# Kernel optimization log

Hardware: AMD Instinct MI355X
Metric: run time of the kernel (lower is better)

Reference implementation:

```python
import jax, jax.numpy as jnp
import numpy as np

N = 200000    # nodes
DMAX = 32     # max in-degree (padded)
F = 128       # in_feats
H = 128       # lstm hidden == in_feats (use_pp=False)
OUT = 128     # out_feats


def setup_inputs() -> dict:
    key = jax.random.key(0)
    ks = jax.random.split(key, 11)
    u = lambda k, shape, s: jax.random.uniform(k, shape, jnp.float32, -s, s)
    feat = jax.random.normal(ks[0], (N, F), jnp.float32)
    # norms come from sqrt(degree) in the original; keep them positive, O(1)
    in_norm = jax.random.uniform(ks[1], (N,), jnp.float32) + 1.0
    out_norm = jax.random.uniform(ks[2], (N,), jnp.float32) + 1.0
    neighbors = jax.random.randint(ks[3], (N, DMAX), 0, N, jnp.int32)
    degrees = jax.random.randint(ks[4], (N,), 1, DMAX + 1, jnp.int32)
    s_lstm = 1.0 / np.sqrt(H)   # torch LSTM default init scale
    s_lin = 1.0 / np.sqrt(F)    # module's reset_parameters scale
    W_ih = u(ks[5], (4 * H, F), s_lstm)
    W_hh = u(ks[6], (4 * H, H), s_lstm)
    b_ih = u(ks[7], (4 * H,), s_lstm)
    b_hh = u(ks[8], (4 * H,), s_lstm)
    W_lin = u(ks[9], (OUT, F), s_lin)
    b_lin = u(ks[10], (OUT,), s_lin)
    return dict(feat=feat, in_norm=in_norm, out_norm=out_norm,
                W_ih=W_ih, W_hh=W_hh, b_ih=b_ih, b_hh=b_hh,
                W_lin=W_lin, b_lin=b_lin,
                neighbors=neighbors, degrees=degrees)


def reference(feat, in_norm, out_norm, W_ih, W_hh, b_ih, b_hh, W_lin, b_lin,
              neighbors, degrees):
    # graph.nodes['_U'].data['h'] = feat / out_norm
    msg_src = feat / out_norm[:, None]                      # [N, F]
    n, dmax = neighbors.shape
    h_dim = W_hh.shape[1]
    step_mask = jnp.arange(dmax)[None, :] < degrees[:, None]  # [N, DMAX]

    def step(carry, xs):
        h, c = carry
        idx_t, m_t = xs                                      # [N], [N]
        x = msg_src[idx_t]                                   # gather messages [N, F]
        gates = x @ W_ih.T + b_ih + h @ W_hh.T + b_hh        # [N, 4H]
        i, f, g, o = jnp.split(gates, 4, axis=-1)
        i = jax.nn.sigmoid(i)
        f = jax.nn.sigmoid(f)
        o = jax.nn.sigmoid(o)
        g = jnp.tanh(g)
        c_new = f * c + i * g
        h_new = o * jnp.tanh(c_new)
        m = m_t[:, None]
        return (jnp.where(m, h_new, h), jnp.where(m, c_new, c)), None

    init = (jnp.zeros((n, h_dim), feat.dtype), jnp.zeros((n, h_dim), feat.dtype))
    (h_final, _), _ = jax.lax.scan(step, init, (neighbors.T, step_mask.T))
    # feat = linear(h / in_norm)
    return (h_final / in_norm[:, None]) @ W_lin.T + b_lin
```

## Files before the change

### kernel.cpp

```cpp
#include <hip/hip_runtime.h>

#define NN 200000
#define NB 64
#define NWG (NN / NB)

typedef unsigned short u16;
typedef unsigned int u32;
typedef __attribute__((ext_vector_type(8))) short short8;
typedef __attribute__((ext_vector_type(4))) float f32x4;

#define LOG2E 1.4426950408889634f
#define TWOLOG2E 2.8853900817779268f

__device__ __forceinline__ u16 f2bf(float x) {
  u32 u = __float_as_uint(x);
  u += 0x7FFFu + ((u >> 16) & 1u);
  return (u16)(u >> 16);
}

typedef __attribute__((address_space(3))) unsigned int lds_u32_t;
typedef const __attribute__((address_space(1))) unsigned int glb_u32_t;
__device__ __forceinline__ void gload16(const void* g, void* l) {
  __builtin_amdgcn_global_load_lds((glb_u32_t*)g, (lds_u32_t*)l, 16, 0, 0);
}

__global__ void k_prep_msg(const float* __restrict__ feat, const float* __restrict__ onorm,
                           u16* __restrict__ msg) {
  int i = blockIdx.x * 256 + threadIdx.x;
  int row = i >> 4, c8 = (i & 15) * 8;
  const float4 a = *(const float4*)(feat + (size_t)row * 128 + c8);
  const float4 b = *(const float4*)(feat + (size_t)row * 128 + c8 + 4);
  float s = 1.0f / onorm[row];
  short8 v = { (short)f2bf(a.x * s), (short)f2bf(a.y * s), (short)f2bf(a.z * s), (short)f2bf(a.w * s),
               (short)f2bf(b.x * s), (short)f2bf(b.y * s), (short)f2bf(b.z * s), (short)f2bf(b.w * s) };
  *(short8*)(msg + (size_t)row * 128 + c8) = v;
}

__global__ void k_prep_w(const float* __restrict__ Wih, const float* __restrict__ Whh,
                         const float* __restrict__ Wlin, const float* __restrict__ bih,
                         const float* __restrict__ bhh, u16* __restrict__ wihb,
                         u16* __restrict__ whhb, u16* __restrict__ wlinb,
                         float* __restrict__ bsum) {
  int i = blockIdx.x * 256 + threadIdx.x;
  if (i < 65536) {
    int gate = i >> 14;
    float s = (gate == 2) ? TWOLOG2E : -LOG2E;
    wihb[i] = f2bf(Wih[i] * s);
  } else if (i < 131072) {
    int j = i - 65536;
    int gate = j >> 14;
    float s = (gate == 2) ? TWOLOG2E : -LOG2E;
    whhb[j] = f2bf(Whh[j] * s);
  } else if (i < 147456) {
    wlinb[i - 131072] = f2bf(Wlin[i - 131072]);
  } else {
    int j = i - 147456;
    float s = ((j >> 7) == 2) ? TWOLOG2E : -LOG2E;
    bsum[j] = (bih[j] + bhh[j]) * s;
  }
}

__global__ void k_hist(const int* __restrict__ degs, int* __restrict__ hist, int n) {
  __shared__ int lh[33];
  if (threadIdx.x < 33) lh[threadIdx.x] = 0;
  __syncthreads();
  int i = blockIdx.x * 256 + threadIdx.x;
  if (i < n) atomicAdd(&lh[degs[i]], 1);
  __syncthreads();
  if (threadIdx.x < 33 && lh[threadIdx.x]) atomicAdd(&hist[threadIdx.x], lh[threadIdx.x]);
}

__global__ void k_scan(const int* __restrict__ hist, int* __restrict__ basep) {
  if (threadIdx.x == 0 && blockIdx.x == 0) {
    int a = 0;
    for (int d = 32; d >= 1; --d) { basep[d] = a; a += hist[d]; }
    basep[0] = a;
  }
}

__global__ void k_scatter(const int* __restrict__ degs, int* __restrict__ basep,
                          int* __restrict__ perm, int n) {
  __shared__ int lh[33], lbase[33], lc[33];
  int t = threadIdx.x;
  if (t < 33) { lh[t] = 0; lc[t] = 0; }
  __syncthreads();
  int i = blockIdx.x * 256 + t;
  int d = (i < n) ? degs[i] : 0;
  if (i < n) atomicAdd(&lh[d], 1);
  __syncthreads();
  if (t < 33 && lh[t]) lbase[t] = atomicAdd(&basep[t], lh[t]);
  __syncthreads();
  if (i < n) { int r = atomicAdd(&lc[d], 1); perm[lbase[d] + r] = i; }
}

__global__ __launch_bounds__(512, 2) void k_main(
    const u16* __restrict__ msg, const u16* __restrict__ wihb,
    const u16* __restrict__ whhb, const u16* __restrict__ wlinb,
    const float* __restrict__ bsum, const float* __restrict__ blin,
    const float* __restrict__ inorm, const int* __restrict__ nbrs,
    const int* __restrict__ degs, const int* __restrict__ perm,
    float* __restrict__ out) {
  __shared__ alignas(16) u16 Xl[2][64 * 128];
  __shared__ alignas(16) u16 Hl[2][64 * 136];
  __shared__ int gidl[64];

  const int tid = threadIdx.x;
  const int w = tid >> 6;
  const int lane = tid & 63;
  const int l15 = lane & 15;
  const int g4 = lane >> 4;
  const int w16 = w * 16;
  const int gr = tid >> 4;
  const int xc8 = (((tid & 15) ^ (gr & 15)) * 8);
  const int wbase = w * 512;
  const int base = blockIdx.x * NB;

  if (tid < NB) gidl[tid] = perm[base + tid];
  {
    u32* hz = (u32*)Hl[0];
#pragma unroll
    for (int s = 0; s < 8; ++s) hz[tid + s * 512] = 0;
    if (tid < 256) hz[tid + 4096] = 0;
  }
  __syncthreads();

  const int gid0 = gidl[gr], gid1 = gidl[gr + 32];
  const int* nb0 = nbrs + (size_t)gid0 * 32;
  const int* nb1 = nbrs + (size_t)gid1 * 32;

  {
    int i0 = nb0[0], i1 = nb1[0];
    gload16(msg + (size_t)i0 * 128 + xc8, &Xl[0][wbase]);
    gload16(msg + (size_t)i1 * 128 + xc8, &Xl[0][4096 + wbase]);
  }
  int ni0 = 0, ni1 = 0;
  if (degs[gidl[0]] > 1) { ni0 = nb0[1]; ni1 = nb1[1]; }

  short8 fih[4][4], fhh[4][4];
#pragma unroll
  for (int g = 0; g < 4; ++g)
#pragma unroll
    for (int kk = 0; kk < 4; ++kk) {
      size_t o = (size_t)(g * 128 + w16 + l15) * 128 + kk * 32 + g4 * 8;
      fih[g][kk] = *(const short8*)(wihb + o);
      fhh[g][kk] = *(const short8*)(whhb + o);
    }
  float bias[4];
#pragma unroll
  for (int g = 0; g < 4; ++g) bias[g] = bsum[g * 128 + w16 + l15];

  u32 dgp[4];
#pragma unroll
  for (int r = 0; r < 4; ++r) {
    u32 p = 0;
#pragma unroll
    for (int q = 0; q < 4; ++q) p |= ((u32)degs[gidl[r * 16 + g4 * 4 + q]]) << (8 * q);
    dgp[r] = p;
  }
  const int maxdeg = degs[gidl[0]];

  int xsw[4];
#pragma unroll
  for (int kk = 0; kk < 4; ++kk) xsw[kk] = ((kk * 4 + g4) ^ l15) * 8;

  float c[4][4] = {};
  u32 hpk[4][2] = {};
  __syncthreads();

  int cur = 0;
  for (int t = 0; t < maxdeg; ++t) {
    const int nxt = cur ^ 1;
    if (t + 1 < maxdeg) {
      gload16(msg + (size_t)ni0 * 128 + xc8, &Xl[nxt][wbase]);
      gload16(msg + (size_t)ni1 * 128 + xc8, &Xl[nxt][4096 + wbase]);
    }
    if (t + 2 < maxdeg) { ni0 = nb0[t + 2]; ni1 = nb1[t + 2]; }

    const u16* Xc = &Xl[cur][0];
    const u16* Hc = &Hl[cur][0];
    u16* Hn = &Hl[nxt][0];

#pragma unroll
    for (int rp = 0; rp < 2; ++rp) {
      f32x4 acc[2][4];
#pragma unroll
      for (int r = 0; r < 2; ++r)
#pragma unroll
        for (int g = 0; g < 4; ++g) acc[r][g] = (f32x4){bias[g], bias[g], bias[g], bias[g]};

#pragma unroll
      for (int rf = 0; rf < 2; ++rf) {
        short8 ax[4];
#pragma unroll
        for (int kk = 0; kk < 4; ++kk)
          ax[kk] = *(const short8*)(&Xc[(rp * 32 + rf * 16 + l15) * 128 + xsw[kk]]);
#pragma unroll
        for (int kk = 0; kk < 4; ++kk)
#pragma unroll
          for (int g = 0; g < 4; ++g)
            acc[rf][g] = __builtin_amdgcn_mfma_f32_16x16x32_bf16(ax[kk], fih[g][kk], acc[rf][g], 0, 0, 0);
      }
#pragma unroll
      for (int rf = 0; rf < 2; ++rf) {
        short8 ah[4];
#pragma unroll
        for (int kk = 0; kk < 4; ++kk)
          ah[kk] = *(const short8*)(&Hc[(rp * 32 + rf * 16 + l15) * 136 + kk * 32 + g4 * 8]);
#pragma unroll
        for (int kk = 0; kk < 4; ++kk)
#pragma unroll
          for (int g = 0; g < 4; ++g)
            acc[rf][g] = __builtin_amdgcn_mfma_f32_16x16x32_bf16(ah[kk], fhh[g][kk], acc[rf][g], 0, 0, 0);
      }

#pragma unroll
      for (int r = 0; r < 2; ++r) {
        const int rr = rp * 2 + r;
#pragma unroll
        for (int q = 0; q < 4; ++q) {
          float ei = __builtin_amdgcn_exp2f(acc[r][0][q]);
          float ef = __builtin_amdgcn_exp2f(acc[r][1][q]);
          float eg = __builtin_amdgcn_exp2f(acc[r][2][q]);
          float eo = __builtin_amdgcn_exp2f(acc[r][3][q]);
          float fv  = __builtin_amdgcn_rcpf(1.0f + ef);
          float rig = __builtin_amdgcn_rcpf((1.0f + ei) * (1.0f + eg));
          float ig  = (eg - 1.0f) * rig;
          float cn  = fv * c[rr][q] + ig;
          float ec  = __builtin_amdgcn_exp2f(cn * TWOLOG2E);
          float rho = __builtin_amdgcn_rcpf((1.0f + eo) * (1.0f + ec));
          float hn  = (ec - 1.0f) * rho;
          bool act = (int)((dgp[rr] >> (8 * q)) & 255u) > t;
          c[rr][q] = act ? cn : c[rr][q];
          u32 word = hpk[rr][q >> 1];
          u16 oldv = (u16)(word >> ((q & 1) * 16));
          u16 nh = act ? f2bf(hn) : oldv;
          hpk[rr][q >> 1] = (q & 1) ? ((word & 0x0000FFFFu) | ((u32)nh << 16))
                                    : ((word & 0xFFFF0000u) | (u32)nh);
          Hn[(rr * 16 + g4 * 4 + q) * 136 + w16 + l15] = nh;
        }
      }
    }
    __syncthreads();
    cur = nxt;
  }

  const u16* Hf = &Hl[cur][0];

  short8 wl[4];
#pragma unroll
  for (int kk = 0; kk < 4; ++kk)
    wl[kk] = *(const short8*)(wlinb + (size_t)(w16 + l15) * 128 + kk * 32 + g4 * 8);
  f32x4 a2[4] = {};
#pragma unroll
  for (int kk = 0; kk < 4; ++kk)
#pragma unroll
    for (int r = 0; r < 4; ++r) {
      short8 ah = *(const short8*)(&Hf[(r * 16 + l15) * 136 + kk * 32 + g4 * 8]);
      a2[r] = __builtin_amdgcn_mfma_f32_16x16x32_bf16(ah, wl[kk], a2[r], 0, 0, 0);
    }
  float blv = blin[w16 + l15];
#pragma unroll
  for (int r = 0; r < 4; ++r)
#pragma unroll
    for (int q = 0; q < 4; ++q) {
      int nl = r * 16 + g4 * 4 + q;
      int g = gidl[nl];
      out[(size_t)g * 128 + w16 + l15] = a2[r][q] / inorm[g] + blv;
    }
}

extern "C" void kernel_launch(void* const* d_in, const int* in_sizes, int n_in,
                              void* d_out, int out_size, void* d_ws, size_t ws_size,
                              hipStream_t stream) {
  const float* feat    = (const float*)d_in[0];
  const float* in_norm = (const float*)d_in[1];
  const float* out_nrm = (const float*)d_in[2];
  const float* W_ih    = (const float*)d_in[3];
  const float* W_hh    = (const float*)d_in[4];
  const float* b_ih    = (const float*)d_in[5];
  const float* b_hh    = (const float*)d_in[6];
  const float* W_lin   = (const float*)d_in[7];
  const float* b_lin   = (const float*)d_in[8];
  const int* neighbors = (const int*)d_in[9];
  const int* degrees   = (const int*)d_in[10];
  float* out = (float*)d_out;

  char* ws = (char*)d_ws;
  u16* msg    = (u16*)(ws);
  u16* wihb   = (u16*)(ws + 51200000);
  u16* whhb   = (u16*)(ws + 51331072);
  u16* wlinb  = (u16*)(ws + 51462144);
  float* bsum = (float*)(ws + 51494912);
  int* perm   = (int*)(ws + 51496960);
  int* hist   = (int*)(ws + 52296960);
  int* basep  = hist + 64;
  if (ws_size < 52297600) return;

  hipMemsetAsync(hist, 0, 64 * 4, stream);
  k_prep_msg<<<12500, 256, 0, stream>>>(feat, out_nrm, msg);
  k_prep_w<<<578, 256, 0, stream>>>(W_ih, W_hh, W_lin, b_ih, b_hh, wihb, whhb, wlinb, bsum);
  k_hist<<<782, 256, 0, stream>>>(degrees, hist, NN);
  k_scan<<<1, 1, 0, stream>>>(hist, basep);
  k_scatter<<<782, 256, 0, stream>>>(degrees, basep, perm, NN);
  k_main<<<NWG, 512, 0, stream>>>(msg, wihb, whhb, wlinb, bsum, b_lin, in_norm,
                                  neighbors, degrees, perm, out);
}
```

Measured before the change: 1.059 ms.

## Split node tile into two half-tiles with independent buffers and per-half max degree

Each 64-node workgroup now runs as two 32-row halves with separate X/H double buffers and separate step counts. The second half stops once its own maximum degree is reached instead of running to the tile-wide maximum. Each half's MFMA block is wrapped in s_setprio raises so waves prioritize matrix work. The cost is an extra barrier per timestep and duplicated code, which raises register and instruction pressure.

```diff
diff --git a/kernel.cpp b/kernel.cpp
--- a/kernel.cpp
+++ b/kernel.cpp
@@ -100,8 +100,10 @@
     const float* __restrict__ inorm, const int* __restrict__ nbrs,
     const int* __restrict__ degs, const int* __restrict__ perm,
     float* __restrict__ out) {
-  __shared__ alignas(16) u16 Xl[2][64 * 128];
-  __shared__ alignas(16) u16 Hl[2][64 * 136];
+  __shared__ alignas(16) u16 XA[2][32 * 128];
+  __shared__ alignas(16) u16 XB[2][32 * 128];
+  __shared__ alignas(16) u16 HA[2][32 * 136];
+  __shared__ alignas(16) u16 HB[2][32 * 136];
   __shared__ int gidl[64];
 
   const int tid = threadIdx.x;
@@ -117,24 +119,22 @@
 
   if (tid < NB) gidl[tid] = perm[base + tid];
   {
-    u32* hz = (u32*)Hl[0];
-#pragma unroll
-    for (int s = 0; s < 8; ++s) hz[tid + s * 512] = 0;
-    if (tid < 256) hz[tid + 4096] = 0;
-  }
-  __syncthreads();
-
-  const int gid0 = gidl[gr], gid1 = gidl[gr + 32];
-  const int* nb0 = nbrs + (size_t)gid0 * 32;
-  const int* nb1 = nbrs + (size_t)gid1 * 32;
-
-  {
-    int i0 = nb0[0], i1 = nb1[0];
-    gload16(msg + (size_t)i0 * 128 + xc8, &Xl[0][wbase]);
-    gload16(msg + (size_t)i1 * 128 + xc8, &Xl[0][4096 + wbase]);
-  }
-  int ni0 = 0, ni1 = 0;
-  if (degs[gidl[0]] > 1) { ni0 = nb0[1]; ni1 = nb1[1]; }
+    u32* a = (u32*)HA[0];
+    u32* b = (u32*)HB[0];
+#pragma unroll
+    for (int s = 0; s < 4; ++s) { a[tid + s * 512] = 0; b[tid + s * 512] = 0; }
+    if (tid < 128) { a[tid + 2048] = 0; b[tid + 2048] = 0; }
+  }
+  __syncthreads();
+
+  const int gidA = gidl[gr], gidB = gidl[32 + gr];
+  const int* nbA = nbrs + (size_t)gidA * 32;
+  const int* nbB = nbrs + (size_t)gidB * 32;
+
+  gload16(msg + (size_t)nbA[0] * 128 + xc8, &XA[0][wbase]);
+  gload16(msg + (size_t)nbB[0] * 128 + xc8, &XB[0][wbase]);
+  int niA = nbA[1];
+  int niB = nbB[1];
 
   short8 fih[4][4], fhh[4][4];
 #pragma unroll
@@ -149,51 +149,53 @@
 #pragma unroll
   for (int g = 0; g < 4; ++g) bias[g] = bsum[g * 128 + w16 + l15];
 
-  u32 dgp[4];
-#pragma unroll
-  for (int r = 0; r < 4; ++r) {
-    u32 p = 0;
-#pragma unroll
-    for (int q = 0; q < 4; ++q) p |= ((u32)degs[gidl[r * 16 + g4 * 4 + q]]) << (8 * q);
-    dgp[r] = p;
-  }
-  const int maxdeg = degs[gidl[0]];
+  u32 dgpA[2], dgpB[2];
+#pragma unroll
+  for (int r = 0; r < 2; ++r) {
+    u32 pa = 0, pb = 0;
+#pragma unroll
+    for (int q = 0; q < 4; ++q) {
+      pa |= ((u32)degs[gidl[r * 16 + g4 * 4 + q]]) << (8 * q);
+      pb |= ((u32)degs[gidl[32 + r * 16 + g4 * 4 + q]]) << (8 * q);
+    }
+    dgpA[r] = pa; dgpB[r] = pb;
+  }
+  const int maxdegA = degs[gidl[0]];
+  const int maxdegB = degs[gidl[32]];
 
   int xsw[4];
 #pragma unroll
   for (int kk = 0; kk < 4; ++kk) xsw[kk] = ((kk * 4 + g4) ^ l15) * 8;
 
-  float c[4][4] = {};
-  u32 hpk[4][2] = {};
-  __syncthreads();
-
-  int cur = 0;
-  for (int t = 0; t < maxdeg; ++t) {
-    const int nxt = cur ^ 1;
-    if (t + 1 < maxdeg) {
-      gload16(msg + (size_t)ni0 * 128 + xc8, &Xl[nxt][wbase]);
-      gload16(msg + (size_t)ni1 * 128 + xc8, &Xl[nxt][4096 + wbase]);
-    }
-    if (t + 2 < maxdeg) { ni0 = nb0[t + 2]; ni1 = nb1[t + 2]; }
-
-    const u16* Xc = &Xl[cur][0];
-    const u16* Hc = &Hl[cur][0];
-    u16* Hn = &Hl[nxt][0];
-
-#pragma unroll
-    for (int rp = 0; rp < 2; ++rp) {
+  float cA[2][4] = {}, cB[2][4] = {};
+  u32 hpkA[2][2] = {}, hpkB[2][2] = {};
+  __syncthreads();
+
+  for (int t = 0; t < maxdegA; ++t) {
+    const int curb = t & 1, nxtb = curb ^ 1;
+
+    {
+      if (t + 1 < maxdegA)
+        gload16(msg + (size_t)niA * 128 + xc8, &XA[nxtb][wbase]);
+      niA = nbA[(t + 2) <= 31 ? (t + 2) : 31];
+
+      const u16* Xc = &XA[curb][0];
+      const u16* Hc = &HA[curb][0];
+      u16* Hn = &HA[nxtb][0];
+
       f32x4 acc[2][4];
 #pragma unroll
       for (int r = 0; r < 2; ++r)
 #pragma unroll
         for (int g = 0; g < 4; ++g) acc[r][g] = (f32x4){bias[g], bias[g], bias[g], bias[g]};
 
+      __builtin_amdgcn_s_setprio(1);
 #pragma unroll
       for (int rf = 0; rf < 2; ++rf) {
         short8 ax[4];
 #pragma unroll
         for (int kk = 0; kk < 4; ++kk)
-          ax[kk] = *(const short8*)(&Xc[(rp * 32 + rf * 16 + l15) * 128 + xsw[kk]]);
+          ax[kk] = *(const short8*)(&Xc[(rf * 16 + l15) * 128 + xsw[kk]]);
 #pragma unroll
         for (int kk = 0; kk < 4; ++kk)
 #pragma unroll
@@ -205,67 +207,139 @@
         short8 ah[4];
 #pragma unroll
         for (int kk = 0; kk < 4; ++kk)
-          ah[kk] = *(const short8*)(&Hc[(rp * 32 + rf * 16 + l15) * 136 + kk * 32 + g4 * 8]);
+          ah[kk] = *(const short8*)(&Hc[(rf * 16 + l15) * 136 + kk * 32 + g4 * 8]);
 #pragma unroll
         for (int kk = 0; kk < 4; ++kk)
 #pragma unroll
           for (int g = 0; g < 4; ++g)
             acc[rf][g] = __builtin_amdgcn_mfma_f32_16x16x32_bf16(ah[kk], fhh[g][kk], acc[rf][g], 0, 0, 0);
       }
-
-#pragma unroll
-      for (int r = 0; r < 2; ++r) {
-        const int rr = rp * 2 + r;
+      __builtin_amdgcn_s_setprio(0);
+
+#pragma unroll
+      for (int rr = 0; rr < 2; ++rr)
 #pragma unroll
         for (int q = 0; q < 4; ++q) {
-          float ei = __builtin_amdgcn_exp2f(acc[r][0][q]);
-          float ef = __builtin_amdgcn_exp2f(acc[r][1][q]);
-          float eg = __builtin_amdgcn_exp2f(acc[r][2][q]);
-          float eo = __builtin_amdgcn_exp2f(acc[r][3][q]);
+          float ei = __builtin_amdgcn_exp2f(acc[rr][0][q]);
+          float ef = __builtin_amdgcn_exp2f(acc[rr][1][q]);
+          float eg = __builtin_amdgcn_exp2f(acc[rr][2][q]);
+          float eo = __builtin_amdgcn_exp2f(acc[rr][3][q]);
           float fv  = __builtin_amdgcn_rcpf(1.0f + ef);
           float rig = __builtin_amdgcn_rcpf((1.0f + ei) * (1.0f + eg));
           float ig  = (eg - 1.0f) * rig;
-          float cn  = fv * c[rr][q] + ig;
+          float cn  = fv * cA[rr][q] + ig;
           float ec  = __builtin_amdgcn_exp2f(cn * TWOLOG2E);
           float rho = __builtin_amdgcn_rcpf((1.0f + eo) * (1.0f + ec));
           float hn  = (ec - 1.0f) * rho;
-          bool act = (int)((dgp[rr] >> (8 * q)) & 255u) > t;
-          c[rr][q] = act ? cn : c[rr][q];
-          u32 word = hpk[rr][q >> 1];
+          bool act = (int)((dgpA[rr] >> (8 * q)) & 255u) > t;
+          cA[rr][q] = act ? cn : cA[rr][q];
+          u32 word = hpkA[rr][q >> 1];
           u16 oldv = (u16)(word >> ((q & 1) * 16));
           u16 nh = act ? f2bf(hn) : oldv;
-          hpk[rr][q >> 1] = (q & 1) ? ((word & 0x0000FFFFu) | ((u32)nh << 16))
-                                    : ((word & 0xFFFF0000u) | (u32)nh);
+          hpkA[rr][q >> 1] = (q & 1) ? ((word & 0x0000FFFFu) | ((u32)nh << 16))
+                                     : ((word & 0xFFFF0000u) | (u32)nh);
           Hn[(rr * 16 + g4 * 4 + q) * 136 + w16 + l15] = nh;
         }
+    }
+    __syncthreads();
+
+    if (t < maxdegB) {
+      if (t + 1 < maxdegB)
+        gload16(msg + (size_t)niB * 128 + xc8, &XB[nxtb][wbase]);
+      niB = nbB[(t + 2) <= 31 ? (t + 2) : 31];
+
+      const u16* Xc = &XB[curb][0];
+      const u16* Hc = &HB[curb][0];
+      u16* Hn = &HB[nxtb][0];
+
+      f32x4 acc[2][4];
+#pragma unroll
+      for (int r = 0; r < 2; ++r)
+#pragma unroll
+        for (int g = 0; g < 4; ++g) acc[r][g] = (f32x4){bias[g], bias[g], bias[g], bias[g]};
+
+      __builtin_amdgcn_s_setprio(1);
+#pragma unroll
+      for (int rf = 0; rf < 2; ++rf) {
+        short8 ax[4];
+#pragma unroll
+        for (int kk = 0; kk < 4; ++kk)
+          ax[kk] = *(const short8*)(&Xc[(rf * 16 + l15) * 128 + xsw[kk]]);
+#pragma unroll
+        for (int kk = 0; kk < 4; ++kk)
+#pragma unroll
+          for (int g = 0; g < 4; ++g)
+            acc[rf][g] = __builtin_amdgcn_mfma_f32_16x16x32_bf16(ax[kk], fih[g][kk], acc[rf][g], 0, 0, 0);
       }
+#pragma unroll
+      for (int rf = 0; rf < 2; ++rf) {
+        short8 ah[4];
+#pragma unroll
+        for (int kk = 0; kk < 4; ++kk)
+          ah[kk] = *(const short8*)(&Hc[(rf * 16 + l15) * 136 + kk * 32 + g4 * 8]);
+#pragma unroll
+        for (int kk = 0; kk < 4; ++kk)
+#pragma unroll
+          for (int g = 0; g < 4; ++g)
+            acc[rf][g] = __builtin_amdgcn_mfma_f32_16x16x32_bf16(ah[kk], fhh[g][kk], acc[rf][g], 0, 0, 0);
+      }
+      __builtin_amdgcn_s_setprio(0);
+
+#pragma unroll
+      for (int rr = 0; rr < 2; ++rr)
+#pragma unroll
+        for (int q = 0; q < 4; ++q) {
+          float ei = __builtin_amdgcn_exp2f(acc[rr][0][q]);
+          float ef = __builtin_amdgcn_exp2f(acc[rr][1][q]);
+          float eg = __builtin_amdgcn_exp2f(acc[rr][2][q]);
+          float eo = __builtin_amdgcn_exp2f(acc[rr][3][q]);
+          float fv  = __builtin_amdgcn_rcpf(1.0f + ef);
+          float rig = __builtin_amdgcn_rcpf((1.0f + ei) * (1.0f + eg));
+          float ig  = (eg - 1.0f) * rig;
+          float cn  = fv * cB[rr][q] + ig;
+          float ec  = __builtin_amdgcn_exp2f(cn * TWOLOG2E);
+          float rho = __builtin_amdgcn_rcpf((1.0f + eo) * (1.0f + ec));
+          float hn  = (ec - 1.0f) * rho;
+          bool act = (int)((dgpB[rr] >> (8 * q)) & 255u) > t;
+          cB[rr][q] = act ? cn : cB[rr][q];
+          u32 word = hpkB[rr][q >> 1];
+          u16 oldv = (u16)(word >> ((q & 1) * 16));
+          u16 nh = act ? f2bf(hn) : oldv;
+          hpkB[rr][q >> 1] = (q & 1) ? ((word & 0x0000FFFFu) | ((u32)nh << 16))
+                                     : ((word & 0xFFFF0000u) | (u32)nh);
+          Hn[(rr * 16 + g4 * 4 + q) * 136 + w16 + l15] = nh;
+        }
     }
     __syncthreads();
-    cur = nxt;
-  }
-
-  const u16* Hf = &Hl[cur][0];
+  }
+
+  const u16* HfA = &HA[maxdegA & 1][0];
+  const u16* HfB = &HB[maxdegB & 1][0];
 
   short8 wl[4];
 #pragma unroll
   for (int kk = 0; kk < 4; ++kk)
     wl[kk] = *(const short8*)(wlinb + (size_t)(w16 + l15) * 128 + kk * 32 + g4 * 8);
-  f32x4 a2[4] = {};
+  f32x4 aA[2] = {}, aB[2] = {};
 #pragma unroll
   for (int kk = 0; kk < 4; ++kk)
 #pragma unroll
-    for (int r = 0; r < 4; ++r) {
-      short8 ah = *(const short8*)(&Hf[(r * 16 + l15) * 136 + kk * 32 + g4 * 8]);
-      a2[r] = __builtin_amdgcn_mfma_f32_16x16x32_bf16(ah, wl[kk], a2[r], 0, 0, 0);
+    for (int r = 0; r < 2; ++r) {
+      short8 hA = *(const short8*)(&HfA[(r * 16 + l15) * 136 + kk * 32 + g4 * 8]);
+      short8 hB = *(const short8*)(&HfB[(r * 16 + l15) * 136 + kk * 32 + g4 * 8]);
+      aA[r] = __builtin_amdgcn_mfma_f32_16x16x32_bf16(hA, wl[kk], aA[r], 0, 0, 0);
+      aB[r] = __builtin_amdgcn_mfma_f32_16x16x32_bf16(hB, wl[kk], aB[r], 0, 0, 0);
     }
   float blv = blin[w16 + l15];
 #pragma unroll
-  for (int r = 0; r < 4; ++r)
+  for (int r = 0; r < 2; ++r)
 #pragma unroll
     for (int q = 0; q < 4; ++q) {
       int nl = r * 16 + g4 * 4 + q;
-      int g = gidl[nl];
-      out[(size_t)g * 128 + w16 + l15] = a2[r][q] / inorm[g] + blv;
+      int gA = gidl[nl];
+      int gB = gidl[32 + nl];
+      out[(size_t)gA * 128 + w16 + l15] = aA[r][q] / inorm[gA] + blv;
+      out[(size_t)gB * 128 + w16 + l15] = aB[r][q] / inorm[gB] + blv;
     }
 }
 
```

Measured after the change: 1.183 ms. +11.7%, slower.

## Replace per-step block barriers with LDS flag counters and triple-buffered gathers

Applied to the files above, without the earlier changes.

Each timestep's __syncthreads is replaced by per-step LDS counters that each of the 8 waves increments after finishing its writes. Waves spin on a flag only when they need the gathered X tile or the previous H tile. The X buffer becomes triple-buffered, with gathers issued two steps ahead, so the input projection for the first half of the rows can start before the previous step's H is complete. MFMA sections are bracketed with s_setprio. This aims to cut barrier stalls and hide gather latency, at the cost of busy-wait spinning and fragile memory-ordering assumptions.

```diff
diff --git a/kernel.cpp b/kernel.cpp
--- a/kernel.cpp
+++ b/kernel.cpp
@@ -22,6 +22,11 @@
 typedef const __attribute__((address_space(1))) unsigned int glb_u32_t;
 __device__ __forceinline__ void gload16(const void* g, void* l) {
   __builtin_amdgcn_global_load_lds((glb_u32_t*)g, (lds_u32_t*)l, 16, 0, 0);
+}
+
+__device__ __forceinline__ void spin8(const volatile int* p) {
+  while (*p < 8) { }
+  asm volatile("" ::: "memory");
 }
 
 __global__ void k_prep_msg(const float* __restrict__ feat, const float* __restrict__ onorm,
@@ -100,9 +105,10 @@
     const float* __restrict__ inorm, const int* __restrict__ nbrs,
     const int* __restrict__ degs, const int* __restrict__ perm,
     float* __restrict__ out) {
-  __shared__ alignas(16) u16 Xl[2][64 * 128];
-  __shared__ alignas(16) u16 Hl[2][64 * 136];
+  __shared__ alignas(16) u16 Xb[3][64 * 128];
+  __shared__ alignas(16) u16 Hb[2][64 * 136];
   __shared__ int gidl[64];
+  __shared__ int fl[72];
 
   const int tid = threadIdx.x;
   const int w = tid >> 6;
@@ -114,10 +120,13 @@
   const int xc8 = (((tid & 15) ^ (gr & 15)) * 8);
   const int wbase = w * 512;
   const int base = blockIdx.x * NB;
+  volatile int* hr = fl;
+  volatile int* xr = fl + 36;
 
   if (tid < NB) gidl[tid] = perm[base + tid];
+  if (tid < 72) fl[tid] = (tid == 0) ? 8 : 0;
   {
-    u32* hz = (u32*)Hl[0];
+    u32* hz = (u32*)Hb[1];
 #pragma unroll
     for (int s = 0; s < 8; ++s) hz[tid + s * 512] = 0;
     if (tid < 256) hz[tid + 4096] = 0;
@@ -128,13 +137,11 @@
   const int* nb0 = nbrs + (size_t)gid0 * 32;
   const int* nb1 = nbrs + (size_t)gid1 * 32;
 
-  {
-    int i0 = nb0[0], i1 = nb1[0];
-    gload16(msg + (size_t)i0 * 128 + xc8, &Xl[0][wbase]);
-    gload16(msg + (size_t)i1 * 128 + xc8, &Xl[0][4096 + wbase]);
-  }
-  int ni0 = 0, ni1 = 0;
-  if (degs[gidl[0]] > 1) { ni0 = nb0[1]; ni1 = nb1[1]; }
+  gload16(msg + (size_t)nb0[0] * 128 + xc8, &Xb[0][wbase]);
+  gload16(msg + (size_t)nb1[0] * 128 + xc8, &Xb[0][4096 + wbase]);
+  gload16(msg + (size_t)nb0[1] * 128 + xc8, &Xb[1][wbase]);
+  gload16(msg + (size_t)nb1[1] * 128 + xc8, &Xb[1][4096 + wbase]);
+  int ni0 = nb0[2], ni1 = nb1[2];
 
   short8 fih[4][4], fhh[4][4];
 #pragma unroll
@@ -165,86 +172,149 @@
 
   float c[4][4] = {};
   u32 hpk[4][2] = {};
-  __syncthreads();
-
-  int cur = 0;
+
+  asm volatile("s_waitcnt vmcnt(0)" ::: "memory");
+  if (lane == 0) { atomicAdd((int*)&xr[0], 1); atomicAdd((int*)&xr[1], 1); }
+
   for (int t = 0; t < maxdeg; ++t) {
-    const int nxt = cur ^ 1;
-    if (t + 1 < maxdeg) {
-      gload16(msg + (size_t)ni0 * 128 + xc8, &Xl[nxt][wbase]);
-      gload16(msg + (size_t)ni1 * 128 + xc8, &Xl[nxt][4096 + wbase]);
-    }
-    if (t + 2 < maxdeg) { ni0 = nb0[t + 2]; ni1 = nb1[t + 2]; }
-
-    const u16* Xc = &Xl[cur][0];
-    const u16* Hc = &Hl[cur][0];
-    u16* Hn = &Hl[nxt][0];
-
-#pragma unroll
-    for (int rp = 0; rp < 2; ++rp) {
-      f32x4 acc[2][4];
-#pragma unroll
-      for (int r = 0; r < 2; ++r)
-#pragma unroll
-        for (int g = 0; g < 4; ++g) acc[r][g] = (f32x4){bias[g], bias[g], bias[g], bias[g]};
-
-#pragma unroll
-      for (int rf = 0; rf < 2; ++rf) {
-        short8 ax[4];
-#pragma unroll
-        for (int kk = 0; kk < 4; ++kk)
-          ax[kk] = *(const short8*)(&Xc[(rp * 32 + rf * 16 + l15) * 128 + xsw[kk]]);
-#pragma unroll
-        for (int kk = 0; kk < 4; ++kk)
-#pragma unroll
-          for (int g = 0; g < 4; ++g)
-            acc[rf][g] = __builtin_amdgcn_mfma_f32_16x16x32_bf16(ax[kk], fih[g][kk], acc[rf][g], 0, 0, 0);
+    const u16* Xc = &Xb[t % 3][0];
+    const u16* Hc = &Hb[(t + 1) & 1][0];
+    u16* Hn = &Hb[t & 1][0];
+
+    spin8(&xr[t]);
+    f32x4 acc[2][4];
+#pragma unroll
+    for (int r = 0; r < 2; ++r)
+#pragma unroll
+      for (int g = 0; g < 4; ++g) acc[r][g] = (f32x4){bias[g], bias[g], bias[g], bias[g]};
+    __builtin_amdgcn_s_setprio(1);
+#pragma unroll
+    for (int rf = 0; rf < 2; ++rf) {
+      short8 ax[4];
+#pragma unroll
+      for (int kk = 0; kk < 4; ++kk)
+        ax[kk] = *(const short8*)(&Xc[(rf * 16 + l15) * 128 + xsw[kk]]);
+#pragma unroll
+      for (int kk = 0; kk < 4; ++kk)
+#pragma unroll
+        for (int g = 0; g < 4; ++g)
+          acc[rf][g] = __builtin_amdgcn_mfma_f32_16x16x32_bf16(ax[kk], fih[g][kk], acc[rf][g], 0, 0, 0);
+    }
+    __builtin_amdgcn_s_setprio(0);
+
+    spin8(&hr[t]);
+
+    if (t + 2 < maxdeg) {
+      gload16(msg + (size_t)ni0 * 128 + xc8, &Xb[(t + 2) % 3][wbase]);
+      gload16(msg + (size_t)ni1 * 128 + xc8, &Xb[(t + 2) % 3][4096 + wbase]);
+    }
+    { int nt = (t + 3) <= 31 ? (t + 3) : 31; ni0 = nb0[nt]; ni1 = nb1[nt]; }
+
+    __builtin_amdgcn_s_setprio(1);
+#pragma unroll
+    for (int rf = 0; rf < 2; ++rf) {
+      short8 ah[4];
+#pragma unroll
+      for (int kk = 0; kk < 4; ++kk)
+        ah[kk] = *(const short8*)(&Hc[(rf * 16 + l15) * 136 + kk * 32 + g4 * 8]);
+#pragma unroll
+      for (int kk = 0; kk < 4; ++kk)
+#pragma unroll
+        for (int g = 0; g < 4; ++g)
+          acc[rf][g] = __builtin_amdgcn_mfma_f32_16x16x32_bf16(ah[kk], fhh[g][kk], acc[rf][g], 0, 0, 0);
+    }
+    __builtin_amdgcn_s_setprio(0);
+#pragma unroll
+    for (int r = 0; r < 2; ++r)
+#pragma unroll
+      for (int q = 0; q < 4; ++q) {
+        float ei = __builtin_amdgcn_exp2f(acc[r][0][q]);
+        float ef = __builtin_amdgcn_exp2f(acc[r][1][q]);
+        float eg = __builtin_amdgcn_exp2f(acc[r][2][q]);
+        float eo = __builtin_amdgcn_exp2f(acc[r][3][q]);
+        float fv  = __builtin_amdgcn_rcpf(1.0f + ef);
+        float rig = __builtin_amdgcn_rcpf((1.0f + ei) * (1.0f + eg));
+        float ig  = (eg - 1.0f) * rig;
+        float cn  = fv * c[r][q] + ig;
+        float ec  = __builtin_amdgcn_exp2f(cn * TWOLOG2E);
+        float rho = __builtin_amdgcn_rcpf((1.0f + eo) * (1.0f + ec));
+        float hn  = (ec - 1.0f) * rho;
+        bool act = (int)((dgp[r] >> (8 * q)) & 255u) > t;
+        c[r][q] = act ? cn : c[r][q];
+        u32 word = hpk[r][q >> 1];
+        u16 oldv = (u16)(word >> ((q & 1) * 16));
+        u16 nh = act ? f2bf(hn) : oldv;
+        hpk[r][q >> 1] = (q & 1) ? ((word & 0x0000FFFFu) | ((u32)nh << 16))
+                                 : ((word & 0xFFFF0000u) | (u32)nh);
+        Hn[(r * 16 + g4 * 4 + q) * 136 + w16 + l15] = nh;
       }
-#pragma unroll
-      for (int rf = 0; rf < 2; ++rf) {
-        short8 ah[4];
-#pragma unroll
-        for (int kk = 0; kk < 4; ++kk)
-          ah[kk] = *(const short8*)(&Hc[(rp * 32 + rf * 16 + l15) * 136 + kk * 32 + g4 * 8]);
-#pragma unroll
-        for (int kk = 0; kk < 4; ++kk)
-#pragma unroll
-          for (int g = 0; g < 4; ++g)
-            acc[rf][g] = __builtin_amdgcn_mfma_f32_16x16x32_bf16(ah[kk], fhh[g][kk], acc[rf][g], 0, 0, 0);
+
+#pragma unroll
+    for (int r = 0; r < 2; ++r)
+#pragma unroll
+      for (int g = 0; g < 4; ++g) acc[r][g] = (f32x4){bias[g], bias[g], bias[g], bias[g]};
+    __builtin_amdgcn_s_setprio(1);
+#pragma unroll
+    for (int rf = 0; rf < 2; ++rf) {
+      short8 ax[4];
+#pragma unroll
+      for (int kk = 0; kk < 4; ++kk)
+        ax[kk] = *(const short8*)(&Xc[(32 + rf * 16 + l15) * 128 + xsw[kk]]);
+#pragma unroll
+      for (int kk = 0; kk < 4; ++kk)
+#pragma unroll
+        for (int g = 0; g < 4; ++g)
+          acc[rf][g] = __builtin_amdgcn_mfma_f32_16x16x32_bf16(ax[kk], fih[g][kk], acc[rf][g], 0, 0, 0);
+    }
+#pragma unroll
+    for (int rf = 0; rf < 2; ++rf) {
+      short8 ah[4];
+#pragma unroll
+      for (int kk = 0; kk < 4; ++kk)
+        ah[kk] = *(const short8*)(&Hc[(32 + rf * 16 + l15) * 136 + kk * 32 + g4 * 8]);
+#pragma unroll
+      for (int kk = 0; kk < 4; ++kk)
+#pragma unroll
+        for (int g = 0; g < 4; ++g)
+          acc[rf][g] = __builtin_amdgcn_mfma_f32_16x16x32_bf16(ah[kk], fhh[g][kk], acc[rf][g], 0, 0, 0);
+    }
+    __builtin_amdgcn_s_setprio(0);
+#pragma unroll
+    for (int r = 0; r < 2; ++r) {
+      const int rr = 2 + r;
+#pragma unroll
+      for (int q = 0; q < 4; ++q) {
+        float ei = __builtin_amdgcn_exp2f(acc[r][0][q]);
+        float ef = __builtin_amdgcn_exp2f(acc[r][1][q]);
+        float eg = __builtin_amdgcn_exp2f(acc[r][2][q]);
+        float eo = __builtin_amdgcn_exp2f(acc[r][3][q]);
+        float fv  = __builtin_amdgcn_rcpf(1.0f + ef);
+        float rig = __builtin_amdgcn_rcpf((1.0f + ei) * (1.0f + eg));
+        float ig  = (eg - 1.0f) * rig;
+        float cn  = fv * c[rr][q] + ig;
+        float ec  = __builtin_amdgcn_exp2f(cn * TWOLOG2E);
+        float rho = __builtin_amdgcn_rcpf((1.0f + eo) * (1.0f + ec));
+        float hn  = (ec - 1.0f) * rho;
+        bool act = (int)((dgp[rr] >> (8 * q)) & 255u) > t;
+        c[rr][q] = act ? cn : c[rr][q];
+        u32 word = hpk[rr][q >> 1];
+        u16 oldv = (u16)(word >> ((q & 1) * 16));
+        u16 nh = act ? f2bf(hn) : oldv;
+        hpk[rr][q >> 1] = (q & 1) ? ((word & 0x0000FFFFu) | ((u32)nh << 16))
+                                  : ((word & 0xFFFF0000u) | (u32)nh);
+        Hn[((rr) * 16 + g4 * 4 + q) * 136 + w16 + l15] = nh;
       }
-
-#pragma unroll
-      for (int r = 0; r < 2; ++r) {
-        const int rr = rp * 2 + r;
-#pragma unroll
-        for (int q = 0; q < 4; ++q) {
-          float ei = __builtin_amdgcn_exp2f(acc[r][0][q]);
-          float ef = __builtin_amdgcn_exp2f(acc[r][1][q]);
-          float eg = __builtin_amdgcn_exp2f(acc[r][2][q]);
-          float eo = __builtin_amdgcn_exp2f(acc[r][3][q]);
-          float fv  = __builtin_amdgcn_rcpf(1.0f + ef);
-          float rig = __builtin_amdgcn_rcpf((1.0f + ei) * (1.0f + eg));
-          float ig  = (eg - 1.0f) * rig;
-          float cn  = fv * c[rr][q] + ig;
-          float ec  = __builtin_amdgcn_exp2f(cn * TWOLOG2E);
-          float rho = __builtin_amdgcn_rcpf((1.0f + eo) * (1.0f + ec));
-          float hn  = (ec - 1.0f) * rho;
-          bool act = (int)((dgp[rr] >> (8 * q)) & 255u) > t;
-          c[rr][q] = act ? cn : c[rr][q];
-          u32 word = hpk[rr][q >> 1];
-          u16 oldv = (u16)(word >> ((q & 1) * 16));
-          u16 nh = act ? f2bf(hn) : oldv;
-          hpk[rr][q >> 1] = (q & 1) ? ((word & 0x0000FFFFu) | ((u32)nh << 16))
-                                    : ((word & 0xFFFF0000u) | (u32)nh);
-          Hn[(rr * 16 + g4 * 4 + q) * 136 + w16 + l15] = nh;
-        }
-      }
-    }
-    __syncthreads();
-    cur = nxt;
-  }
-
-  const u16* Hf = &Hl[cur][0];
+    }
+
+    asm volatile("s_waitcnt vmcnt(0) lgkmcnt(0)" ::: "memory");
+    if (lane == 0) {
+      atomicAdd((int*)&hr[t + 1], 1);
+      atomicAdd((int*)&xr[t + 2], 1);
+    }
+  }
+
+  spin8(&hr[maxdeg]);
+  const u16* Hf = &Hb[(maxdeg - 1) & 1][0];
 
   short8 wl[4];
 #pragma unroll
```

Result: faster. 1.020 ms (median of 2 runs) (-3.7%).
